# Kernel optimization log

Measured on AMD Instinct MI355X. Metric: run time of the kernel, lower is better.

## Reference

```python
import jax, jax.numpy as jnp
import numpy as np

G, K_ORD = 5, 3          # efficient-kan defaults: grid_size=5, spline_order=3
NB = G + K_ORD           # 8 spline basis functions per input feature
H, NH, S, B = 1024, 16, 1024, 2
HD = H // NH
DFF, E, TOPK = 1024, 4, 2


def b_splines(x):
    # x: [..., in] -> bases: [..., in, NB]; uniform grid on [-1,1] extended by K_ORD knots
    h = 2.0 / G
    grid = jnp.arange(-K_ORD, G + K_ORD + 1, dtype=x.dtype) * h - 1.0  # [G+2k+1]=12
    xg = x[..., None]
    bases = ((xg >= grid[:-1]) & (xg < grid[1:])).astype(x.dtype)      # order-0
    for j in range(1, K_ORD + 1):  # Cox-de Boor recursion
        left = (xg - grid[:-(j + 1)]) / (grid[j:-1] - grid[:-(j + 1)]) * bases[..., :-1]
        right = (grid[j + 1:] - xg) / (grid[j + 1:] - grid[1:-j]) * bases[..., 1:]
        bases = left + right
    return bases  # [..., in, NB]


def kan_linear(x, base_w, spline_w, scaler):
    # base path: SiLU(x) @ W_base^T ; spline path: B(x) contracted with scaled spline weights
    base = jax.nn.silu(x) @ base_w.T                       # [..., out]
    sw = spline_w * scaler[..., None]                      # [out, in, NB]
    spline = jnp.einsum('...ic,oic->...o', b_splines(x), sw)
    return base + spline


def rmsnorm(x, w, eps=1e-6):
    return w * (x * jax.lax.rsqrt(jnp.mean(x * x, axis=-1, keepdims=True) + eps))


def ffn(x, b1, s1, c1, b2, s2, c2, b3, s3, c3):
    # linear3(linear1(x) * linear2(x)), all KANLinear
    return kan_linear(kan_linear(x, b1, s1, c1) * kan_linear(x, b2, s2, c2), b3, s3, c3)


def setup_inputs() -> dict:
    key = jax.random.key(0)
    ks = jax.random.split(key, 24)
    sc = 0.02
    d = {}
    d['x'] = jax.random.normal(ks[0], (B, S, H), jnp.float32)
    inv_freq = 1.0 / (10000.0 ** (np.arange(0, HD, 2, dtype=np.float32) / HD))
    ang = np.arange(S, dtype=np.float32)[:, None] * inv_freq[None, :]  # [S, HD//2]
    d['rot_cos'] = jnp.asarray(np.cos(ang))
    d['rot_sin'] = jnp.asarray(np.sin(ang))
    d['norm1_w'] = jnp.ones((H,), jnp.float32)
    d['norm2_w'] = jnp.ones((H,), jnp.float32)
    d['qkv_base'] = jax.random.normal(ks[1], (3 * H, H), jnp.float32) * sc
    d['qkv_spline'] = jax.random.normal(ks[2], (3 * H, H, NB), jnp.float32) * sc
    d['qkv_scaler'] = jax.random.normal(ks[3], (3 * H, H), jnp.float32) * sc + 1.0
    d['out_w'] = jax.random.normal(ks[4], (H, H), jnp.float32) * sc
    d['out_b'] = jnp.zeros((H,), jnp.float32)
    d['gate_w'] = jax.random.normal(ks[5], (E, H), jnp.float32) * sc
    # stacked expert params (vmapped over E)
    d['w1_base'] = jax.random.normal(ks[6], (E, DFF, H), jnp.float32) * sc
    d['w1_spline'] = jax.random.normal(ks[7], (E, DFF, H, NB), jnp.float32) * sc
    d['w1_scaler'] = jax.random.normal(ks[8], (E, DFF, H), jnp.float32) * sc + 1.0
    d['w2_base'] = jax.random.normal(ks[9], (E, DFF, H), jnp.float32) * sc
    d['w2_spline'] = jax.random.normal(ks[10], (E, DFF, H, NB), jnp.float32) * sc
    d['w2_scaler'] = jax.random.normal(ks[11], (E, DFF, H), jnp.float32) * sc + 1.0
    d['w3_base'] = jax.random.normal(ks[12], (E, H, DFF), jnp.float32) * sc
    d['w3_spline'] = jax.random.normal(ks[13], (E, H, DFF, NB), jnp.float32) * sc
    d['w3_scaler'] = jax.random.normal(ks[14], (E, H, DFF), jnp.float32) * sc + 1.0
    return d


def reference(x, rot_cos, rot_sin, norm1_w, norm2_w, qkv_base, qkv_spline, qkv_scaler,
              out_w, out_b, gate_w, w1_base, w1_spline, w1_scaler, w2_base, w2_spline,
              w2_scaler, w3_base, w3_spline, w3_scaler):
    b, s, h = x.shape
    # ---- attention branch ----
    hn = rmsnorm(x, norm1_w)
    qkv = kan_linear(hn, qkv_base, qkv_spline, qkv_scaler)          # [B,S,3H]
    qkv = qkv.reshape(b, s, NH, 3 * HD).transpose(0, 2, 1, 3)       # [B,NH,S,3HD]
    q, k, v = jnp.split(qkv, 3, axis=-1)                            # [B,NH,S,HD]

    def rope(t):
        tr = t.reshape(b, NH, s, HD // 2, 2)
        re, im = tr[..., 0], tr[..., 1]
        c, sn = rot_cos[:s], rot_sin[:s]                            # [S,HD//2]
        nre = re * c - im * sn
        nim = re * sn + im * c
        return jnp.stack([nre, nim], axis=-1).reshape(b, NH, s, HD)

    q, k = rope(q), rope(k)
    scores = jnp.einsum('bhqd,bhkd->bhqk', q, k) / (HD ** 0.5)
    attn = jax.nn.softmax(scores, axis=-1)
    ctx = jnp.einsum('bhqk,bhkd->bhqd', attn, v)
    ctx = ctx.transpose(0, 2, 1, 3).reshape(b, s, h)
    x = x + ctx @ out_w.T + out_b

    # ---- MoE-KAN FFN branch ----
    h2 = rmsnorm(x, norm2_w)
    gate_logits = h2 @ gate_w.T                                     # [B,S,E]
    w_top, sel = jax.lax.top_k(gate_logits, TOPK)                   # [B,S,K]
    w_top = jax.nn.softmax(w_top.astype(jnp.float32), axis=-1).astype(x.dtype)
    # run every expert densely (same math as masked dispatch), then gather top-k
    y_all = jax.vmap(
        lambda b1, s1, c1, b2, s2, c2, b3, s3, c3:
            ffn(h2, b1, s1, c1, b2, s2, c2, b3, s3, c3)
    )(w1_base, w1_spline, w1_scaler, w2_base, w2_spline, w2_scaler,
      w3_base, w3_spline, w3_scaler)                                # [E,B,S,H]
    y_bseh = jnp.transpose(y_all, (1, 2, 0, 3))                     # [B,S,E,H]
    gathered = jnp.take_along_axis(y_bseh, sel[..., None], axis=2)  # [B,S,K,H]
    moe_out = jnp.sum(w_top[..., None] * gathered, axis=2)          # [B,S,H]
    return x + moe_out
```

## Files before the change

### kernel.cpp

```cpp
#include <hip/hip_runtime.h>
#include <hip/hip_bf16.h>

#define T_TOK 2048
#define H_DIM 1024
#define S_SEQ 1024
#define NHEAD 16
#define E_EXP 4
#define DFF_  1024
#define KAUG  9216

typedef __bf16 bf16x8 __attribute__((ext_vector_type(8)));
typedef float  f32x4  __attribute__((ext_vector_type(4)));
typedef unsigned short ushort_t;

__device__ __forceinline__ float sigmoidf_(float x) { return 1.0f / (1.0f + __expf(-x)); }

__device__ __forceinline__ unsigned short f2bf(float f) {
    unsigned int u = __float_as_uint(f);
    u = (u + 0x7fffu + ((u >> 16) & 1u)) >> 16;
    return (unsigned short)u;
}
__device__ __forceinline__ float bf2f(unsigned short h) {
    return __uint_as_float(((unsigned int)h) << 16);
}

__device__ __forceinline__ void bspline8(float x, float* o) {
    float b[11];
#pragma unroll
    for (int m = 0; m < 11; ++m) {
        float g0 = 0.4f * (float)(m - 3) - 1.0f;
        float g1 = 0.4f * (float)(m - 2) - 1.0f;
        b[m] = (x >= g0 && x < g1) ? 1.0f : 0.0f;
    }
#pragma unroll
    for (int j = 1; j <= 3; ++j) {
        float inv = 1.0f / (0.4f * (float)j);
#pragma unroll
        for (int m = 0; m + j < 11; ++m) {
            float gm   = 0.4f * (float)(m - 3) - 1.0f;
            float gmj1 = 0.4f * (float)(m + j - 2) - 1.0f;
            b[m] = ((x - gm) * b[m] + (gmj1 - x) * b[m + 1]) * inv;
        }
    }
#pragma unroll
    for (int c = 0; c < 8; ++c) o[c] = b[c];
}

__global__ __launch_bounds__(256) void rmsnorm_kernel(const float* __restrict__ x,
                                                      const float* __restrict__ w,
                                                      float* __restrict__ out) {
    long t = blockIdx.x;
    float4 v = ((const float4*)(x + t * H_DIM))[threadIdx.x];
    float ss = v.x * v.x + v.y * v.y + v.z * v.z + v.w * v.w;
#pragma unroll
    for (int m = 1; m < 64; m <<= 1) ss += __shfl_xor(ss, m, 64);
    __shared__ float wsum[4];
    if ((threadIdx.x & 63) == 0) wsum[threadIdx.x >> 6] = ss;
    __syncthreads();
    ss = wsum[0] + wsum[1] + wsum[2] + wsum[3];
    float sc = rsqrtf(ss * (1.0f / (float)H_DIM) + 1e-6f);
    float4 wv = ((const float4*)w)[threadIdx.x];
    float4 r;
    r.x = v.x * sc * wv.x; r.y = v.y * sc * wv.y;
    r.z = v.z * sc * wv.z; r.w = v.w * sc * wv.w;
    ((float4*)(out + t * H_DIM))[threadIdx.x] = r;
}

__global__ __launch_bounds__(256) void pack_act(const float* __restrict__ act,
                                                ushort_t* __restrict__ hi,
                                                ushort_t* __restrict__ lo) {
    long idx = (long)blockIdx.x * 256 + threadIdx.x;
    long m = idx >> 10; int i = (int)(idx & 1023);
    float v = act[idx];
    float ch[9];
    ch[0] = v * sigmoidf_(v);
    bspline8(v, ch + 1);
    ushort_t* oh = hi + m * (long)KAUG + i;
#pragma unroll
    for (int c = 0; c < 9; ++c) oh[(long)c * 1024] = f2bf(ch[c]);
    if (lo) {
        ushort_t* ol = lo + m * (long)KAUG + i;
#pragma unroll
        for (int c = 0; c < 9; ++c) {
            unsigned short h = f2bf(ch[c]);
            ol[(long)c * 1024] = f2bf(ch[c] - bf2f(h));
        }
    }
}

__global__ __launch_bounds__(256) void pack_w(const float* __restrict__ base,
                                              const float* __restrict__ spl,
                                              const float* __restrict__ scal,
                                              ushort_t* __restrict__ hi,
                                              ushort_t* __restrict__ lo,
                                              long total) {
    long idx = (long)blockIdx.x * 256 + threadIdx.x;
    if (idx >= total) return;
    long n = idx >> 10; int i = (int)(idx & 1023);
    float sc = scal[idx];
    const float4* s4 = (const float4*)(spl + idx * 8);
    float4 s0 = s4[0], s1 = s4[1];
    float ch[9] = {base[idx], s0.x * sc, s0.y * sc, s0.z * sc, s0.w * sc,
                   s1.x * sc, s1.y * sc, s1.z * sc, s1.w * sc};
    ushort_t* oh = hi + n * (long)KAUG + i;
#pragma unroll
    for (int c = 0; c < 9; ++c) oh[(long)c * 1024] = f2bf(ch[c]);
    if (lo) {
        ushort_t* ol = lo + n * (long)KAUG + i;
#pragma unroll
        for (int c = 0; c < 9; ++c) {
            unsigned short h = f2bf(ch[c]);
            ol[(long)c * 1024] = f2bf(ch[c] - bf2f(h));
        }
    }
}

__global__ __launch_bounds__(256) void mul_pack4(const float* __restrict__ g1,
                                                 const float* __restrict__ g2,
                                                 ushort_t* __restrict__ G) {
    long idx = (long)blockIdx.x * 256 + threadIdx.x;
    long t = idx >> 12; int ei = (int)(idx & 4095);
    int e = ei >> 10, i = ei & 1023;
    float v = g1[idx] * g2[idx];
    float ch[9];
    ch[0] = v * sigmoidf_(v);
    bspline8(v, ch + 1);
    ushort_t* oh = G + ((long)e * T_TOK + t) * (long)KAUG + i;
#pragma unroll
    for (int c = 0; c < 9; ++c) oh[(long)c * 1024] = f2bf(ch[c]);
}

__global__ __launch_bounds__(256) void split_pack(const float* __restrict__ in,
                                                  ushort_t* __restrict__ hi,
                                                  ushort_t* __restrict__ lo, long n) {
    long i = (long)blockIdx.x * 256 + threadIdx.x;
    if (i >= n) return;
    float v = in[i];
    unsigned short h = f2bf(v);
    hi[i] = h;
    lo[i] = f2bf(v - bf2f(h));
}

#define GLD(gp, lp) __builtin_amdgcn_global_load_lds( \
    (const __attribute__((address_space(1))) void*)(gp), \
    (__attribute__((address_space(3))) void*)(lp), 16, 0, 0)

template<int BM, int SPLIT, int MODE>
__global__ __launch_bounds__(256) void mfma_gemm2(const ushort_t* __restrict__ Ah,
                                                  const ushort_t* __restrict__ Al,
                                                  const ushort_t* __restrict__ Bh,
                                                  const ushort_t* __restrict__ Bl,
                                                  float* __restrict__ C,
                                                  const float* __restrict__ rowScale,
                                                  const float* __restrict__ bias,
                                                  const float* __restrict__ res,
                                                  int N, int K) {
    constexpr int NM = BM / 32;
    __shared__ __align__(16) ushort_t AsH[BM * 32];
    __shared__ __align__(16) ushort_t BsH[128 * 32];
    __shared__ __align__(16) ushort_t AsL[SPLIT ? BM * 32 : 16];
    __shared__ __align__(16) ushort_t BsL[SPLIT ? 128 * 32 : 16];
    const int nx = gridDim.x;
    const int nwg = nx * gridDim.y;
    const int bid = blockIdx.y * nx + blockIdx.x;
    const int q8 = nwg >> 3, r8 = nwg & 7;
    const int xc = bid & 7, dd = bid >> 3;
    const int nid = (xc < r8 ? xc * (q8 + 1) : r8 * (q8 + 1) + (xc - r8) * q8) + dd;
    const int bm = (nid / nx) * BM, bn = (nid % nx) * 128;

    const ushort_t* Ap = Ah;
    const ushort_t* Bp = Bh;
    const float* rsp = rowScale;
    if constexpr (MODE == 3) {
        Ap  += (size_t)blockIdx.z * (size_t)gridDim.y * BM * (size_t)K;
        Bp  += (size_t)blockIdx.z * (size_t)N * (size_t)K;
        rsp += blockIdx.z;
    }

    const int tid = threadIdx.x;
    const int w = tid >> 6, l = tid & 63;
    const int wr = w >> 1, wc = w & 1;
    const int half = l >> 4, lr = l & 15;
    const size_t rb = (size_t)K * 2;

    const int rowB0 = w * 32 + (l >> 2), rowB1 = rowB0 + 16;
    const int cch = l & 3;
    const char* gB0 = (const char*)Bp + (size_t)(bn + rowB0) * rb + ((cch ^ (rowB0 & 3)) * 16);
    const char* gB1 = (const char*)Bp + (size_t)(bn + rowB1) * rb + ((cch ^ (rowB1 & 3)) * 16);
    const char* gB0l = SPLIT ? (const char*)Bl + (size_t)(bn + rowB0) * rb + ((cch ^ (rowB0 & 3)) * 16) : nullptr;
    const char* gB1l = SPLIT ? (const char*)Bl + (size_t)(bn + rowB1) * rb + ((cch ^ (rowB1 & 3)) * 16) : nullptr;
    int rowA0, rowA1;
    if constexpr (BM == 128) { rowA0 = w * 32 + (l >> 2); rowA1 = rowA0 + 16; }
    else                     { rowA0 = w * 16 + (l >> 2); rowA1 = 0; }
    const char* gA0 = (const char*)Ap + (size_t)(bm + rowA0) * rb + ((cch ^ (rowA0 & 3)) * 16);
    const char* gA1 = (BM == 128) ? (const char*)Ap + (size_t)(bm + rowA1) * rb + ((cch ^ (rowA1 & 3)) * 16) : nullptr;
    const char* gA0l = SPLIT ? (const char*)Al + (size_t)(bm + rowA0) * rb + ((cch ^ (rowA0 & 3)) * 16) : nullptr;
    const char* gA1l = (SPLIT && BM == 128) ? (const char*)Al + (size_t)(bm + rowA1) * rb + ((cch ^ (rowA1 & 3)) * 16) : nullptr;

    f32x4 acc[NM][4] = {};
    for (int k0 = 0; k0 < K; k0 += 32) {
        const size_t kb = (size_t)k0 * 2;
        GLD(gA0 + kb, (char*)AsH + ((BM == 128) ? w * 2048 : w * 1024) + l * 16);
        if constexpr (BM == 128) GLD(gA1 + kb, (char*)AsH + w * 2048 + 1024 + l * 16);
        GLD(gB0 + kb, (char*)BsH + w * 2048 + l * 16);
        GLD(gB1 + kb, (char*)BsH + w * 2048 + 1024 + l * 16);
        if constexpr (SPLIT) {
            GLD(gA0l + kb, (char*)AsL + ((BM == 128) ? w * 2048 : w * 1024) + l * 16);
            if constexpr (BM == 128) GLD(gA1l + kb, (char*)AsL + w * 2048 + 1024 + l * 16);
            GLD(gB0l + kb, (char*)BsL + w * 2048 + l * 16);
            GLD(gB1l + kb, (char*)BsL + w * 2048 + 1024 + l * 16);
        }
        __syncthreads();
        bf16x8 ah[NM], bh[4];
#pragma unroll
        for (int mi = 0; mi < NM; ++mi) {
            int r = wr * (BM / 2) + mi * 16 + lr;
            ah[mi] = *(const bf16x8*)((const char*)AsH + r * 64 + ((half ^ (r & 3)) * 16));
        }
#pragma unroll
        for (int ni = 0; ni < 4; ++ni) {
            int r = wc * 64 + ni * 16 + lr;
            bh[ni] = *(const bf16x8*)((const char*)BsH + r * 64 + ((half ^ (r & 3)) * 16));
        }
#pragma unroll
        for (int mi = 0; mi < NM; ++mi)
#pragma unroll
            for (int ni = 0; ni < 4; ++ni)
                acc[mi][ni] = __builtin_amdgcn_mfma_f32_16x16x32_bf16(ah[mi], bh[ni],
                                                                      acc[mi][ni], 0, 0, 0);
        if constexpr (SPLIT) {
            bf16x8 al[NM], bl[4];
#pragma unroll
            for (int mi = 0; mi < NM; ++mi) {
                int r = wr * (BM / 2) + mi * 16 + lr;
                al[mi] = *(const bf16x8*)((const char*)AsL + r * 64 + ((half ^ (r & 3)) * 16));
            }
#pragma unroll
            for (int ni = 0; ni < 4; ++ni) {
                int r = wc * 64 + ni * 16 + lr;
                bl[ni] = *(const bf16x8*)((const char*)BsL + r * 64 + ((half ^ (r & 3)) * 16));
            }
#pragma unroll
            for (int mi = 0; mi < NM; ++mi)
#pragma unroll
                for (int ni = 0; ni < 4; ++ni) {
                    acc[mi][ni] = __builtin_amdgcn_mfma_f32_16x16x32_bf16(ah[mi], bl[ni],
                                                                          acc[mi][ni], 0, 0, 0);
                    acc[mi][ni] = __builtin_amdgcn_mfma_f32_16x16x32_bf16(al[mi], bh[ni],
                                                                          acc[mi][ni], 0, 0, 0);
                }
        }
        __syncthreads();
    }
#pragma unroll
    for (int mi = 0; mi < NM; ++mi)
#pragma unroll
        for (int r = 0; r < 4; ++r) {
            int row = bm + wr * (BM / 2) + mi * 16 + half * 4 + r;
            float rs = (MODE == 1 || MODE == 3) ? rsp[(size_t)row * 4] : 0.0f;
#pragma unroll
            for (int ni = 0; ni < 4; ++ni) {
                int col = bn + wc * 64 + ni * 16 + lr;
                size_t ix = (size_t)row * N + col;
                if constexpr (MODE == 0)      C[ix] = acc[mi][ni][r];
                else if constexpr (MODE == 1) C[ix] += rs * acc[mi][ni][r];
                else if constexpr (MODE == 2) C[ix] = res[ix] + bias[col] + acc[mi][ni][r];
                else                          unsafeAtomicAdd(&C[ix], rs * acc[mi][ni][r]);
            }
        }
}

__global__ __launch_bounds__(256) void qk_pack(const float* __restrict__ qkv,
                                               const float* __restrict__ cs,
                                               const float* __restrict__ sn,
                                               ushort_t* __restrict__ Qh, ushort_t* __restrict__ Ql,
                                               ushort_t* __restrict__ Kh, ushort_t* __restrict__ Kl) {
    int idx = blockIdx.x * 256 + threadIdx.x;
    int p = idx & 31;
    int h = (idx >> 5) & 15;
    int s = (idx >> 9) & (S_SEQ - 1);
    int b = idx >> 19;
    float c = cs[s * 32 + p], si = sn[s * 32 + p];
    long base = ((long)(b * S_SEQ + s)) * 3072 + h * 192;
    long dst = (((long)(b * NHEAD + h)) * S_SEQ + s) * 64 + 2 * p;
    float re = qkv[base + 2 * p], im = qkv[base + 2 * p + 1];
    float qre = (re * c - im * si) * 0.125f;
    float qim = (re * si + im * c) * 0.125f;
    unsigned short hh = f2bf(qre);
    Qh[dst] = hh; Ql[dst] = f2bf(qre - bf2f(hh));
    hh = f2bf(qim);
    Qh[dst + 1] = hh; Ql[dst + 1] = f2bf(qim - bf2f(hh));
    re = qkv[base + 64 + 2 * p]; im = qkv[base + 64 + 2 * p + 1];
    float kre = re * c - im * si;
    float kim = re * si + im * c;
    hh = f2bf(kre);
    Kh[dst] = hh; Kl[dst] = f2bf(kre - bf2f(hh));
    hh = f2bf(kim);
    Kh[dst + 1] = hh; Kl[dst + 1] = f2bf(kim - bf2f(hh));
}

__global__ __launch_bounds__(256) void v_trans(const float* __restrict__ qkv,
                                               ushort_t* __restrict__ Vth,
                                               ushort_t* __restrict__ Vtl) {
    __shared__ float t[64][65];
    const int s0 = blockIdx.x * 64, h = blockIdx.y, b = blockIdx.z;
    const int tid = threadIdx.x;
#pragma unroll
    for (int i = 0; i < 16; ++i) {
        int e = tid + i * 256;
        int sl = e >> 6, d = e & 63;
        t[d][sl] = qkv[((long)(b * S_SEQ + s0 + sl)) * 3072 + h * 192 + 128 + d];
    }
    __syncthreads();
#pragma unroll
    for (int i = 0; i < 16; ++i) {
        int e = tid + i * 256;
        int d = e >> 6, sl = e & 63;
        float v = t[d][sl];
        long o = (((long)(b * NHEAD + h)) * 64 + d) * S_SEQ + s0 + sl;
        unsigned short hh = f2bf(v);
        Vth[o] = hh;
        Vtl[o] = f2bf(v - bf2f(hh));
    }
}

__device__ __forceinline__ bf16x8 lds_frag(const ushort_t* base, int row, int chunk) {
    return *(const bf16x8*)((const char*)base + row * 128 + ((chunk ^ (row & 7)) * 16));
}

__global__ __launch_bounds__(256) void attn_mfma(const ushort_t* __restrict__ Qh,
                                                 const ushort_t* __restrict__ Ql,
                                                 const ushort_t* __restrict__ Kh,
                                                 const ushort_t* __restrict__ Kl,
                                                 const ushort_t* __restrict__ Vth,
                                                 const ushort_t* __restrict__ Vtl,
                                                 float* __restrict__ ctx) {
    __shared__ __align__(16) ushort_t KsH[64 * 64], KsL[64 * 64];
    __shared__ __align__(16) ushort_t VsH[64 * 64], VsL[64 * 64];
    __shared__ __align__(16) ushort_t Ps[4][2][16][72];
    const int qb = blockIdx.x * 64, h = blockIdx.y, b = blockIdx.z;
    const int tid = threadIdx.x;
    const int w = tid >> 6, l = tid & 63;
    const int lr = l & 15, g = l >> 4;
    const long bh = b * NHEAD + h;

    const long qoff = (bh * S_SEQ + qb + w * 16 + lr) * 64 + g * 8;
    bf16x8 qh0 = *(const bf16x8*)(Qh + qoff);
    bf16x8 qh1 = *(const bf16x8*)(Qh + qoff + 32);
    bf16x8 ql0 = *(const bf16x8*)(Ql + qoff);
    bf16x8 ql1 = *(const bf16x8*)(Ql + qoff + 32);

    const int rowS0 = w * 16 + (l >> 3), rowS1 = rowS0 + 8;
    const int cch = l & 7;
    const char* gK0 = (const char*)Kh + (bh * S_SEQ + rowS0) * 128 + ((cch ^ (rowS0 & 7)) * 16);
    const char* gK1 = (const char*)Kh + (bh * S_SEQ + rowS1) * 128 + ((cch ^ (rowS1 & 7)) * 16);
    const char* gKl0 = (const char*)Kl + (bh * S_SEQ + rowS0) * 128 + ((cch ^ (rowS0 & 7)) * 16);
    const char* gKl1 = (const char*)Kl + (bh * S_SEQ + rowS1) * 128 + ((cch ^ (rowS1 & 7)) * 16);
    const char* gV0 = (const char*)Vth + (bh * 64 + rowS0) * 2048 + ((cch ^ (rowS0 & 7)) * 16);
    const char* gV1 = (const char*)Vth + (bh * 64 + rowS1) * 2048 + ((cch ^ (rowS1 & 7)) * 16);
    const char* gVl0 = (const char*)Vtl + (bh * 64 + rowS0) * 2048 + ((cch ^ (rowS0 & 7)) * 16);
    const char* gVl1 = (const char*)Vtl + (bh * 64 + rowS1) * 2048 + ((cch ^ (rowS1 & 7)) * 16);

    float m_run[4] = {-1e30f, -1e30f, -1e30f, -1e30f};
    float l_run[4] = {0.f, 0.f, 0.f, 0.f};
    f32x4 acco[4] = {};

    for (int k0 = 0; k0 < S_SEQ; k0 += 64) {
        GLD(gK0 + (size_t)k0 * 128, (char*)KsH + w * 2048 + l * 16);
        GLD(gK1 + (size_t)k0 * 128, (char*)KsH + w * 2048 + 1024 + l * 16);
        GLD(gKl0 + (size_t)k0 * 128, (char*)KsL + w * 2048 + l * 16);
        GLD(gKl1 + (size_t)k0 * 128, (char*)KsL + w * 2048 + 1024 + l * 16);
        GLD(gV0 + (size_t)k0 * 2, (char*)VsH + w * 2048 + l * 16);
        GLD(gV1 + (size_t)k0 * 2, (char*)VsH + w * 2048 + 1024 + l * 16);
        GLD(gVl0 + (size_t)k0 * 2, (char*)VsL + w * 2048 + l * 16);
        GLD(gVl1 + (size_t)k0 * 2, (char*)VsL + w * 2048 + 1024 + l * 16);
        __syncthreads();

        f32x4 accs[4] = {};
#pragma unroll
        for (int n = 0; n < 4; ++n) {
            bf16x8 bkh0 = lds_frag(KsH, n * 16 + lr, g);
            bf16x8 bkh1 = lds_frag(KsH, n * 16 + lr, g + 4);
            bf16x8 bkl0 = lds_frag(KsL, n * 16 + lr, g);
            bf16x8 bkl1 = lds_frag(KsL, n * 16 + lr, g + 4);
            accs[n] = __builtin_amdgcn_mfma_f32_16x16x32_bf16(qh0, bkh0, accs[n], 0, 0, 0);
            accs[n] = __builtin_amdgcn_mfma_f32_16x16x32_bf16(qh1, bkh1, accs[n], 0, 0, 0);
            accs[n] = __builtin_amdgcn_mfma_f32_16x16x32_bf16(qh0, bkl0, accs[n], 0, 0, 0);
            accs[n] = __builtin_amdgcn_mfma_f32_16x16x32_bf16(qh1, bkl1, accs[n], 0, 0, 0);
            accs[n] = __builtin_amdgcn_mfma_f32_16x16x32_bf16(ql0, bkh0, accs[n], 0, 0, 0);
            accs[n] = __builtin_amdgcn_mfma_f32_16x16x32_bf16(ql1, bkh1, accs[n], 0, 0, 0);
        }
        float alpha[4];
#pragma unroll
        for (int r = 0; r < 4; ++r) {
            float mx = fmaxf(fmaxf(accs[0][r], accs[1][r]), fmaxf(accs[2][r], accs[3][r]));
#pragma unroll
            for (int msk = 1; msk < 16; msk <<= 1) mx = fmaxf(mx, __shfl_xor(mx, msk, 64));
            float m_new = fmaxf(m_run[r], mx);
            float ps = 0.f;
#pragma unroll
            for (int n = 0; n < 4; ++n) {
                float p = __expf(accs[n][r] - m_new);
                accs[n][r] = p;
                ps += p;
            }
#pragma unroll
            for (int msk = 1; msk < 16; msk <<= 1) ps += __shfl_xor(ps, msk, 64);
            alpha[r] = __expf(m_run[r] - m_new);
            l_run[r] = l_run[r] * alpha[r] + ps;
            m_run[r] = m_new;
        }
#pragma unroll
        for (int nd = 0; nd < 4; ++nd)
#pragma unroll
            for (int r = 0; r < 4; ++r) acco[nd][r] *= alpha[r];
#pragma unroll
        for (int n = 0; n < 4; ++n)
#pragma unroll
            for (int r = 0; r < 4; ++r) {
                float p = accs[n][r];
                unsigned short hh = f2bf(p);
                Ps[w][0][g * 4 + r][n * 16 + lr] = hh;
                Ps[w][1][g * 4 + r][n * 16 + lr] = f2bf(p - bf2f(hh));
            }
        __syncthreads();
        bf16x8 pah0 = *(const bf16x8*)&Ps[w][0][lr][g * 8];
        bf16x8 pah1 = *(const bf16x8*)&Ps[w][0][lr][32 + g * 8];
        bf16x8 pal0 = *(const bf16x8*)&Ps[w][1][lr][g * 8];
        bf16x8 pal1 = *(const bf16x8*)&Ps[w][1][lr][32 + g * 8];
#pragma unroll
        for (int nd = 0; nd < 4; ++nd) {
            bf16x8 bvh0 = lds_frag(VsH, nd * 16 + lr, g);
            bf16x8 bvh1 = lds_frag(VsH, nd * 16 + lr, g + 4);
            bf16x8 bvl0 = lds_frag(VsL, nd * 16 + lr, g);
            bf16x8 bvl1 = lds_frag(VsL, nd * 16 + lr, g + 4);
            acco[nd] = __builtin_amdgcn_mfma_f32_16x16x32_bf16(pah0, bvh0, acco[nd], 0, 0, 0);
            acco[nd] = __builtin_amdgcn_mfma_f32_16x16x32_bf16(pah1, bvh1, acco[nd], 0, 0, 0);
            acco[nd] = __builtin_amdgcn_mfma_f32_16x16x32_bf16(pah0, bvl0, acco[nd], 0, 0, 0);
            acco[nd] = __builtin_amdgcn_mfma_f32_16x16x32_bf16(pah1, bvl1, acco[nd], 0, 0, 0);
            acco[nd] = __builtin_amdgcn_mfma_f32_16x16x32_bf16(pal0, bvh0, acco[nd], 0, 0, 0);
            acco[nd] = __builtin_amdgcn_mfma_f32_16x16x32_bf16(pal1, bvh1, acco[nd], 0, 0, 0);
        }
        __syncthreads();
    }
#pragma unroll
    for (int r = 0; r < 4; ++r) {
        float inv = 1.0f / l_run[r];
        long row = (long)b * S_SEQ + qb + w * 16 + g * 4 + r;
#pragma unroll
        for (int nd = 0; nd < 4; ++nd)
            ctx[row * H_DIM + h * 64 + nd * 16 + lr] = acco[nd][r] * inv;
    }
}

__global__ __launch_bounds__(256) void gate_kernel(const float* __restrict__ h2,
                                                   const float* __restrict__ gate_w,
                                                   float* __restrict__ gw) {
    long t = blockIdx.x;
    float sum[4] = {0, 0, 0, 0};
    for (int i = threadIdx.x; i < H_DIM; i += 256) {
        float v = h2[t * H_DIM + i];
#pragma unroll
        for (int e = 0; e < 4; ++e) sum[e] = fmaf(v, gate_w[e * H_DIM + i], sum[e]);
    }
#pragma unroll
    for (int w = 1; w < 64; w <<= 1)
#pragma unroll
        for (int e = 0; e < 4; ++e) sum[e] += __shfl_xor(sum[e], w, 64);
    __shared__ float part[4][4];
    if ((threadIdx.x & 63) == 0)
#pragma unroll
        for (int e = 0; e < 4; ++e) part[e][threadIdx.x >> 6] = sum[e];
    __syncthreads();
    if (threadIdx.x == 0) {
        float lg[4];
#pragma unroll
        for (int e = 0; e < 4; ++e) lg[e] = part[e][0] + part[e][1] + part[e][2] + part[e][3];
        int i0 = 0;
        for (int e = 1; e < 4; ++e) if (lg[e] > lg[i0]) i0 = e;
        int i1 = -1;
        for (int e = 0; e < 4; ++e) if (e != i0 && (i1 < 0 || lg[e] > lg[i1])) i1 = e;
        float mx = fmaxf(lg[i0], lg[i1]);
        float e0 = __expf(lg[i0] - mx), e1 = __expf(lg[i1] - mx);
        float inv = 1.0f / (e0 + e1);
        float o[4] = {0, 0, 0, 0};
        o[i0] = e0 * inv; o[i1] = e1 * inv;
#pragma unroll
        for (int e = 0; e < 4; ++e) gw[t * 4 + e] = o[e];
    }
}

#define KI 8
#define BKK 72
__global__ __launch_bounds__(256) void kan_gemm(const float* __restrict__ Act,
                                                const float* __restrict__ baseW,
                                                const float* __restrict__ splW,
                                                const float* __restrict__ scal,
                                                float* __restrict__ C,
                                                const float* __restrict__ rowScale,
                                                int rsStride, int N, int mode) {
    __shared__ float As[BKK][64];
    __shared__ float Bs[BKK][64];
    const int bm = blockIdx.y * 64;
    const int bn = blockIdx.x * 64;
    const int tid = threadIdx.x;
    const int tx = tid & 15, ty = tid >> 4;
    float acc[4][4] = {};
    for (int i0 = 0; i0 < H_DIM; i0 += KI) {
        for (int e = tid; e < 64 * KI; e += 256) {
            int m = e >> 3, ii = e & 7;
            float xv = Act[(long)(bm + m) * H_DIM + i0 + ii];
            float sp[8];
            bspline8(xv, sp);
            As[ii * 9][m] = xv * sigmoidf_(xv);
#pragma unroll
            for (int c = 0; c < 8; ++c) As[ii * 9 + 1 + c][m] = sp[c];
        }
        for (int e = tid; e < 64 * KI; e += 256) {
            int n = e >> 3, ii = e & 7;
            long w = (long)(bn + n) * H_DIM + i0 + ii;
            float sc = scal[w];
            Bs[ii * 9][n] = baseW[w];
            const float4* sp4 = (const float4*)(splW + w * 8);
            float4 s0 = sp4[0], s1 = sp4[1];
            Bs[ii * 9 + 1][n] = s0.x * sc; Bs[ii * 9 + 2][n] = s0.y * sc;
            Bs[ii * 9 + 3][n] = s0.z * sc; Bs[ii * 9 + 4][n] = s0.w * sc;
            Bs[ii * 9 + 5][n] = s1.x * sc; Bs[ii * 9 + 6][n] = s1.y * sc;
            Bs[ii * 9 + 7][n] = s1.z * sc; Bs[ii * 9 + 8][n] = s1.w * sc;
        }
        __syncthreads();
#pragma unroll 8
        for (int k = 0; k < BKK; ++k) {
            float4 a = *(const float4*)&As[k][ty * 4];
            float4 b = *(const float4*)&Bs[k][tx * 4];
            float av[4] = {a.x, a.y, a.z, a.w};
            float bv[4] = {b.x, b.y, b.z, b.w};
#pragma unroll
            for (int i = 0; i < 4; ++i)
#pragma unroll
                for (int j = 0; j < 4; ++j) acc[i][j] = fmaf(av[i], bv[j], acc[i][j]);
        }
        __syncthreads();
    }
#pragma unroll
    for (int i = 0; i < 4; ++i) {
        long m = bm + ty * 4 + i;
        float rs = (mode == 1) ? rowScale[m * rsStride] : 0.0f;
#pragma unroll
        for (int j = 0; j < 4; ++j) {
            long idx = m * (long)N + bn + tx * 4 + j;
            if (mode == 0) C[idx] = acc[i][j];
            else           C[idx] += rs * acc[i][j];
        }
    }
}

__global__ __launch_bounds__(256) void gemm_bias_res(const float* __restrict__ A,
                                                     const float* __restrict__ Bw,
                                                     const float* __restrict__ bias,
                                                     const float* __restrict__ res,
                                                     float* __restrict__ C) {
    __shared__ float As[16][64];
    __shared__ float Bs[16][64];
    const int bm = blockIdx.y * 64, bn = blockIdx.x * 64;
    const int tid = threadIdx.x;
    const int tx = tid & 15, ty = tid >> 4;
    float acc[4][4] = {};
    for (int k0 = 0; k0 < 1024; k0 += 16) {
        for (int e = tid; e < 1024; e += 256) {
            int r = e >> 4, kk = e & 15;
            As[kk][r] = A[(long)(bm + r) * 1024 + k0 + kk];
            Bs[kk][r] = Bw[(long)(bn + r) * 1024 + k0 + kk];
        }
        __syncthreads();
#pragma unroll
        for (int k = 0; k < 16; ++k) {
            float4 a = *(const float4*)&As[k][ty * 4];
            float4 b = *(const float4*)&Bs[k][tx * 4];
            float av[4] = {a.x, a.y, a.z, a.w};
            float bv[4] = {b.x, b.y, b.z, b.w};
#pragma unroll
            for (int i = 0; i < 4; ++i)
#pragma unroll
                for (int j = 0; j < 4; ++j) acc[i][j] = fmaf(av[i], bv[j], acc[i][j]);
        }
        __syncthreads();
    }
#pragma unroll
    for (int i = 0; i < 4; ++i) {
        long m = bm + ty * 4 + i;
#pragma unroll
        for (int j = 0; j < 4; ++j) {
            long n = bn + tx * 4 + j;
            C[m * 1024 + n] = res[m * 1024 + n] + bias[n] + acc[i][j];
        }
    }
}

__global__ __launch_bounds__(256) void rope_kernel(float* __restrict__ qkv,
                                                   const float* __restrict__ cs,
                                                   const float* __restrict__ sn) {
    int idx = blockIdx.x * 256 + threadIdx.x;
    if (idx >= T_TOK * NHEAD * 32) return;
    int p = idx & 31;
    int n = (idx >> 5) & 15;
    int t = idx >> 9;
    int s = t & (S_SEQ - 1);
    float c = cs[s * 32 + p], si = sn[s * 32 + p];
    long base = (long)t * 3072 + n * 192;
    float re = qkv[base + 2 * p], im = qkv[base + 2 * p + 1];
    qkv[base + 2 * p]     = re * c - im * si;
    qkv[base + 2 * p + 1] = re * si + im * c;
    re = qkv[base + 64 + 2 * p]; im = qkv[base + 64 + 2 * p + 1];
    qkv[base + 64 + 2 * p]     = re * c - im * si;
    qkv[base + 64 + 2 * p + 1] = re * si + im * c;
}

__global__ __launch_bounds__(256) void attn_kernel(const float* __restrict__ qkv,
                                                   float* __restrict__ ctx) {
    const int qb = blockIdx.x * 32;
    const int h = blockIdx.y, b = blockIdx.z;
    __shared__ float Qs[32][64];
    __shared__ float Ks[64][64];
    __shared__ float Vs[64][64];
    __shared__ float Ss[32][64];
    const int tid = threadIdx.x;
    const int q = tid >> 3, g = tid & 7;
    for (int e = tid; e < 32 * 64; e += 256) {
        int r = e >> 6, d = e & 63;
        Qs[r][d] = qkv[(long)(b * S_SEQ + qb + r) * 3072 + h * 192 + d];
    }
    float m_run = -1e30f, l_run = 0.0f;
    float acc[8] = {};
    for (int k0 = 0; k0 < S_SEQ; k0 += 64) {
        for (int e = tid; e < 64 * 64; e += 256) {
            int r = e >> 6, d = e & 63;
            long base = (long)(b * S_SEQ + k0 + r) * 3072 + h * 192;
            Ks[r][d] = qkv[base + 64 + d];
            Vs[r][d] = qkv[base + 128 + d];
        }
        __syncthreads();
        float s[8];
#pragma unroll
        for (int kk = 0; kk < 8; ++kk) {
            int k = g * 8 + kk;
            float dot = 0.0f;
#pragma unroll
            for (int d = 0; d < 64; ++d) dot = fmaf(Qs[q][d], Ks[k][d], dot);
            s[kk] = dot * 0.125f;
        }
        float mx = s[0];
#pragma unroll
        for (int kk = 1; kk < 8; ++kk) mx = fmaxf(mx, s[kk]);
#pragma unroll
        for (int w = 1; w < 8; w <<= 1) mx = fmaxf(mx, __shfl_xor(mx, w, 64));
        float m_new = fmaxf(m_run, mx);
        float p[8], ls = 0.0f;
#pragma unroll
        for (int kk = 0; kk < 8; ++kk) { p[kk] = __expf(s[kk] - m_new); ls += p[kk]; }
#pragma unroll
        for (int w = 1; w < 8; w <<= 1) ls += __shfl_xor(ls, w, 64);
        float alpha = __expf(m_run - m_new);
        l_run = l_run * alpha + ls;
        m_run = m_new;
#pragma unroll
        for (int kk = 0; kk < 8; ++kk) Ss[q][g * 8 + kk] = p[kk];
        __syncthreads();
#pragma unroll
        for (int j = 0; j < 8; ++j) acc[j] *= alpha;
        for (int k = 0; k < 64; ++k) {
            float pv = Ss[q][k];
#pragma unroll
            for (int j = 0; j < 8; ++j) acc[j] = fmaf(pv, Vs[k][g * 8 + j], acc[j]);
        }
        __syncthreads();
    }
    float inv = 1.0f / l_run;
#pragma unroll
    for (int j = 0; j < 8; ++j)
        ctx[(long)(b * S_SEQ + qb + q) * H_DIM + h * 64 + g * 8 + j] = acc[j] * inv;
}

__global__ __launch_bounds__(256) void mul_kernel(const float* __restrict__ a,
                                                  const float* __restrict__ b,
                                                  float* __restrict__ c, int n) {
    int i = blockIdx.x * 256 + threadIdx.x;
    if (i < n) c[i] = a[i] * b[i];
}

extern "C" void kernel_launch(void* const* d_in, const int* in_sizes, int n_in,
                              void* d_out, int out_size, void* d_ws, size_t ws_size,
                              hipStream_t stream) {
    const float* x          = (const float*)d_in[0];
    const float* rot_cos    = (const float*)d_in[1];
    const float* rot_sin    = (const float*)d_in[2];
    const float* norm1_w    = (const float*)d_in[3];
    const float* norm2_w    = (const float*)d_in[4];
    const float* qkv_base   = (const float*)d_in[5];
    const float* qkv_spline = (const float*)d_in[6];
    const float* qkv_scaler = (const float*)d_in[7];
    const float* out_w      = (const float*)d_in[8];
    const float* out_b      = (const float*)d_in[9];
    const float* gate_w     = (const float*)d_in[10];
    const float* w1_base    = (const float*)d_in[11];
    const float* w1_spline  = (const float*)d_in[12];
    const float* w1_scaler  = (const float*)d_in[13];
    const float* w2_base    = (const float*)d_in[14];
    const float* w2_spline  = (const float*)d_in[15];
    const float* w2_scaler  = (const float*)d_in[16];
    const float* w3_base    = (const float*)d_in[17];
    const float* w3_spline  = (const float*)d_in[18];
    const float* w3_scaler  = (const float*)d_in[19];
    float* out = (float*)d_out;

    const size_t SZ_AUG  = (size_t)T_TOK * KAUG * 2;
    const size_t SZ_WQ   = (size_t)3072 * KAUG * 2;
    const size_t SZ_QKV  = (size_t)T_TOK * 3072 * 4;
    const size_t SZ_G12  = (size_t)T_TOK * 2048 * 4;
    const size_t SZ_TOK  = (size_t)T_TOK * H_DIM * 4;
    const size_t NEED = 2 * SZ_AUG + 2 * SZ_WQ + SZ_QKV + SZ_G12 + 2 * SZ_TOK + 32768;

    if (ws_size >= NEED) {
        char* pool = (char*)d_ws;
        ushort_t* A_hi = (ushort_t*)pool;
        ushort_t* A_lo = (ushort_t*)(pool + SZ_AUG);
        char* W1p = pool + 2 * SZ_AUG;
        char* W2p = pool + 2 * SZ_AUG + SZ_WQ;
        float* qkv = (float*)(pool + 2 * SZ_AUG + 2 * SZ_WQ);
        float* ctx = (float*)(pool + 2 * SZ_AUG + 2 * SZ_WQ + SZ_QKV + SZ_G12);
        float* tok = (float*)(pool + 2 * SZ_AUG + 2 * SZ_WQ + SZ_QKV + SZ_G12 + SZ_TOK);
        float* gw  = (float*)(pool + NEED - 32768);
        ushort_t* W1b = (ushort_t*)W1p;
        ushort_t* W2b = (ushort_t*)W2p;
        const size_t SZ_P = (size_t)T_TOK * 1024 * 2;
        ushort_t* Qh  = (ushort_t*)W1p;
        ushort_t* Ql  = (ushort_t*)(W1p + SZ_P);
        ushort_t* Kh  = (ushort_t*)(W1p + 2 * SZ_P);
        ushort_t* Kl  = (ushort_t*)(W1p + 3 * SZ_P);
        ushort_t* Vth = (ushort_t*)(W1p + 4 * SZ_P);
        ushort_t* Vtl = (ushort_t*)(W1p + 5 * SZ_P);
        ushort_t* CtxH = (ushort_t*)W2p;
        ushort_t* CtxL = (ushort_t*)(W2p + SZ_P);
        ushort_t* OWh  = (ushort_t*)(W2p + 2 * SZ_P);
        ushort_t* OWl  = (ushort_t*)(W2p + 2 * SZ_P + SZ_P / 2);
        const size_t SZ_G4 = (size_t)T_TOK * 4096 * 4;
        ushort_t* A2   = (ushort_t*)pool;
        ushort_t* W12  = (ushort_t*)(pool + SZ_AUG);
        float*    g1a  = (float*)(pool + NEED - 32768 - 2 * SZ_G4);
        float*    g2a  = (float*)(pool + NEED - 32768 - SZ_G4);
        ushort_t* Gall = (ushort_t*)pool;
        ushort_t* W3a  = (ushort_t*)(pool + 4 * SZ_AUG);

        rmsnorm_kernel<<<T_TOK, 256, 0, stream>>>(x, norm1_w, tok);
        pack_act<<<(T_TOK * 1024) / 256, 256, 0, stream>>>(tok, A_hi, A_lo);
        pack_w<<<(3072 * 1024) / 256, 256, 0, stream>>>(qkv_base, qkv_spline, qkv_scaler,
                                                        W1b, W2b, (long)3072 * 1024);
        mfma_gemm2<128, 1, 0><<<dim3(3072 / 128, T_TOK / 128), 256, 0, stream>>>(
            A_hi, A_lo, W1b, W2b, qkv, nullptr, nullptr, nullptr, 3072, KAUG);
        qk_pack<<<(T_TOK * NHEAD * 32) / 256, 256, 0, stream>>>(qkv, rot_cos, rot_sin,
                                                                Qh, Ql, Kh, Kl);
        v_trans<<<dim3(S_SEQ / 64, NHEAD, 2), 256, 0, stream>>>(qkv, Vth, Vtl);
        attn_mfma<<<dim3(S_SEQ / 64, NHEAD, 2), 256, 0, stream>>>(Qh, Ql, Kh, Kl,
                                                                  Vth, Vtl, ctx);
        split_pack<<<(T_TOK * 1024) / 256, 256, 0, stream>>>(ctx, CtxH, CtxL,
                                                             (long)T_TOK * 1024);
        split_pack<<<(1024 * 1024) / 256, 256, 0, stream>>>(out_w, OWh, OWl,
                                                            (long)1024 * 1024);
        mfma_gemm2<128, 1, 2><<<dim3(1024 / 128, T_TOK / 128), 256, 0, stream>>>(
            CtxH, CtxL, OWh, OWl, out, nullptr, out_b, x, 1024, 1024);
        rmsnorm_kernel<<<T_TOK, 256, 0, stream>>>(out, norm2_w, tok);
        gate_kernel<<<T_TOK, 256, 0, stream>>>(tok, gate_w, gw);

        pack_act<<<(T_TOK * 1024) / 256, 256, 0, stream>>>(tok, A2, nullptr);
        pack_w<<<(4 * 1024 * 1024) / 256, 256, 0, stream>>>(
            w1_base, w1_spline, w1_scaler, W12, nullptr, (long)4 * 1024 * 1024);
        mfma_gemm2<128, 0, 0><<<dim3(4096 / 128, T_TOK / 128), 256, 0, stream>>>(
            A2, nullptr, W12, nullptr, g1a, nullptr, nullptr, nullptr, 4096, KAUG);
        pack_w<<<(4 * 1024 * 1024) / 256, 256, 0, stream>>>(
            w2_base, w2_spline, w2_scaler, W12, nullptr, (long)4 * 1024 * 1024);
        mfma_gemm2<128, 0, 0><<<dim3(4096 / 128, T_TOK / 128), 256, 0, stream>>>(
            A2, nullptr, W12, nullptr, g2a, nullptr, nullptr, nullptr, 4096, KAUG);
        mul_pack4<<<(T_TOK * 4096) / 256, 256, 0, stream>>>(g1a, g2a, Gall);
        pack_w<<<(4 * 1024 * 1024) / 256, 256, 0, stream>>>(
            w3_base, w3_spline, w3_scaler, W3a, nullptr, (long)4 * 1024 * 1024);
        mfma_gemm2<128, 0, 3><<<dim3(1024 / 128, T_TOK / 128, E_EXP), 256, 0, stream>>>(
            Gall, nullptr, W3a, nullptr, out, gw, nullptr, nullptr, 1024, KAUG);
        return;
    }

    char* ws = (char*)d_ws;
    float* hn  = (float*)ws; ws += (size_t)T_TOK * H_DIM * 4;
    float* qkv = (float*)ws; ws += (size_t)T_TOK * 3072 * 4;
    float* ctx = (float*)ws; ws += (size_t)T_TOK * H_DIM * 4;
    float* h2  = (float*)ws; ws += (size_t)T_TOK * H_DIM * 4;
    float* gw  = (float*)ws; ws += (size_t)T_TOK * E_EXP * 4;
    float* g1  = (float*)ws; ws += (size_t)T_TOK * DFF_ * 4;
    float* g2  = (float*)ws; ws += (size_t)T_TOK * DFF_ * 4;
    float* gm  = (float*)ws; ws += (size_t)T_TOK * DFF_ * 4;

    rmsnorm_kernel<<<T_TOK, 256, 0, stream>>>(x, norm1_w, hn);
    dim3 gq(3072 / 64, T_TOK / 64);
    kan_gemm<<<gq, 256, 0, stream>>>(hn, qkv_base, qkv_spline, qkv_scaler, qkv,
                                     nullptr, 0, 3072, 0);
    rope_kernel<<<(T_TOK * NHEAD * 32) / 256, 256, 0, stream>>>(qkv, rot_cos, rot_sin);
    dim3 ga(S_SEQ / 32, NHEAD, 2);
    attn_kernel<<<ga, 256, 0, stream>>>(qkv, ctx);
    dim3 go(1024 / 64, T_TOK / 64);
    gemm_bias_res<<<go, 256, 0, stream>>>(ctx, out_w, out_b, x, out);
    rmsnorm_kernel<<<T_TOK, 256, 0, stream>>>(out, norm2_w, h2);
    gate_kernel<<<T_TOK, 256, 0, stream>>>(h2, gate_w, gw);
    dim3 ge(1024 / 64, T_TOK / 64);
    for (int e = 0; e < E_EXP; ++e) {
        long wo = (long)e * DFF_ * H_DIM;
        kan_gemm<<<ge, 256, 0, stream>>>(h2, w1_base + wo, w1_spline + wo * 8,
                                         w1_scaler + wo, g1, nullptr, 0, DFF_, 0);
        kan_gemm<<<ge, 256, 0, stream>>>(h2, w2_base + wo, w2_spline + wo * 8,
                                         w2_scaler + wo, g2, nullptr, 0, DFF_, 0);
        mul_kernel<<<(T_TOK * DFF_) / 256, 256, 0, stream>>>(g1, g2, gm, T_TOK * DFF_);
        kan_gemm<<<ge, 256, 0, stream>>>(gm, w3_base + wo, w3_spline + wo * 8,
                                         w3_scaler + wo, out, gw + e, E_EXP, H_DIM, 1);
    }
}
```

Measured before the change: 1.588 ms.

## Split-K GEMMs with atomics, merge W1/W2 GEMM with bf16 output

Adds a KSPLIT template parameter so the QKV, out-projection and expert-W3 GEMMs split the K dimension across grid z and accumulate with atomic adds. This raises workgroup counts on the small-N GEMMs, which underfill the GPU. The W1 and W2 expert GEMMs are merged into one N=8192 launch that writes bf16 outputs, and mul_pack4 reads those bf16 values, halving intermediate traffic. The XCD-aware block remapping is removed, and a prefill kernel plus a memset replace the fused bias/residual epilogue. The costs are atomic traffic, extra zero/prefill passes and bf16 rounding of the g1/g2 intermediates.

```diff
diff --git a/kernel.cpp b/kernel.cpp
--- a/kernel.cpp
+++ b/kernel.cpp
@@ -64,6 +64,17 @@
     r.x = v.x * sc * wv.x; r.y = v.y * sc * wv.y;
     r.z = v.z * sc * wv.z; r.w = v.w * sc * wv.w;
     ((float4*)(out + t * H_DIM))[threadIdx.x] = r;
+}
+
+__global__ __launch_bounds__(256) void prefill_out(const float* __restrict__ x,
+                                                   const float* __restrict__ bias,
+                                                   float* __restrict__ out) {
+    long i = (long)blockIdx.x * 256 + threadIdx.x;
+    float4 xv = ((const float4*)x)[i];
+    float4 bv = ((const float4*)bias)[i & 255];
+    float4 r;
+    r.x = xv.x + bv.x; r.y = xv.y + bv.y; r.z = xv.z + bv.z; r.w = xv.w + bv.w;
+    ((float4*)out)[i] = r;
 }
 
 __global__ __launch_bounds__(256) void pack_act(const float* __restrict__ act,
@@ -115,13 +126,14 @@
     }
 }
 
-__global__ __launch_bounds__(256) void mul_pack4(const float* __restrict__ g1,
-                                                 const float* __restrict__ g2,
+__global__ __launch_bounds__(256) void mul_pack4(const ushort_t* __restrict__ g12,
                                                  ushort_t* __restrict__ G) {
     long idx = (long)blockIdx.x * 256 + threadIdx.x;
     long t = idx >> 12; int ei = (int)(idx & 4095);
     int e = ei >> 10, i = ei & 1023;
-    float v = g1[idx] * g2[idx];
+    float g1 = bf2f(g12[t * 8192 + ei]);
+    float g2 = bf2f(g12[t * 8192 + 4096 + ei]);
+    float v = g1 * g2;
     float ch[9];
     ch[0] = v * sigmoidf_(v);
     bspline8(v, ch + 1);
@@ -145,37 +157,32 @@
     (const __attribute__((address_space(1))) void*)(gp), \
     (__attribute__((address_space(3))) void*)(lp), 16, 0, 0)
 
-template<int BM, int SPLIT, int MODE>
+template<int BM, int SPLIT, int MODE, int KSPLIT>
 __global__ __launch_bounds__(256) void mfma_gemm2(const ushort_t* __restrict__ Ah,
                                                   const ushort_t* __restrict__ Al,
                                                   const ushort_t* __restrict__ Bh,
                                                   const ushort_t* __restrict__ Bl,
                                                   float* __restrict__ C,
                                                   const float* __restrict__ rowScale,
-                                                  const float* __restrict__ bias,
-                                                  const float* __restrict__ res,
                                                   int N, int K) {
     constexpr int NM = BM / 32;
     __shared__ __align__(16) ushort_t AsH[BM * 32];
     __shared__ __align__(16) ushort_t BsH[128 * 32];
     __shared__ __align__(16) ushort_t AsL[SPLIT ? BM * 32 : 16];
     __shared__ __align__(16) ushort_t BsL[SPLIT ? 128 * 32 : 16];
-    const int nx = gridDim.x;
-    const int nwg = nx * gridDim.y;
-    const int bid = blockIdx.y * nx + blockIdx.x;
-    const int q8 = nwg >> 3, r8 = nwg & 7;
-    const int xc = bid & 7, dd = bid >> 3;
-    const int nid = (xc < r8 ? xc * (q8 + 1) : r8 * (q8 + 1) + (xc - r8) * q8) + dd;
-    const int bm = (nid / nx) * BM, bn = (nid % nx) * 128;
-
-    const ushort_t* Ap = Ah;
-    const ushort_t* Bp = Bh;
-    const float* rsp = rowScale;
-    if constexpr (MODE == 3) {
-        Ap  += (size_t)blockIdx.z * (size_t)gridDim.y * BM * (size_t)K;
-        Bp  += (size_t)blockIdx.z * (size_t)N * (size_t)K;
-        rsp += blockIdx.z;
-    }
+    const int bm = blockIdx.y * BM, bn = blockIdx.x * 128;
+
+    const int KC = K / KSPLIT;
+    int e = 0, kk = 0;
+    if constexpr (MODE == 3) { e = blockIdx.z / KSPLIT; kk = blockIdx.z % KSPLIT; }
+    else if constexpr (KSPLIT > 1) { kk = blockIdx.z; }
+    const ushort_t* Ap = Ah + (MODE == 3 ? (size_t)e * (size_t)gridDim.y * BM * K : 0)
+                            + (size_t)kk * KC;
+    const ushort_t* Bp = Bh + (MODE == 3 ? (size_t)e * (size_t)N * K : 0)
+                            + (size_t)kk * KC;
+    const ushort_t* Alp = SPLIT ? Al + (size_t)kk * KC : nullptr;
+    const ushort_t* Blp = SPLIT ? Bl + (size_t)kk * KC : nullptr;
+    const float* rsp = rowScale + (MODE == 3 ? e : 0);
 
     const int tid = threadIdx.x;
     const int w = tid >> 6, l = tid & 63;
@@ -187,18 +194,18 @@
     const int cch = l & 3;
     const char* gB0 = (const char*)Bp + (size_t)(bn + rowB0) * rb + ((cch ^ (rowB0 & 3)) * 16);
     const char* gB1 = (const char*)Bp + (size_t)(bn + rowB1) * rb + ((cch ^ (rowB1 & 3)) * 16);
-    const char* gB0l = SPLIT ? (const char*)Bl + (size_t)(bn + rowB0) * rb + ((cch ^ (rowB0 & 3)) * 16) : nullptr;
-    const char* gB1l = SPLIT ? (const char*)Bl + (size_t)(bn + rowB1) * rb + ((cch ^ (rowB1 & 3)) * 16) : nullptr;
+    const char* gB0l = SPLIT ? (const char*)Blp + (size_t)(bn + rowB0) * rb + ((cch ^ (rowB0 & 3)) * 16) : nullptr;
+    const char* gB1l = SPLIT ? (const char*)Blp + (size_t)(bn + rowB1) * rb + ((cch ^ (rowB1 & 3)) * 16) : nullptr;
     int rowA0, rowA1;
     if constexpr (BM == 128) { rowA0 = w * 32 + (l >> 2); rowA1 = rowA0 + 16; }
     else                     { rowA0 = w * 16 + (l >> 2); rowA1 = 0; }
     const char* gA0 = (const char*)Ap + (size_t)(bm + rowA0) * rb + ((cch ^ (rowA0 & 3)) * 16);
     const char* gA1 = (BM == 128) ? (const char*)Ap + (size_t)(bm + rowA1) * rb + ((cch ^ (rowA1 & 3)) * 16) : nullptr;
-    const char* gA0l = SPLIT ? (const char*)Al + (size_t)(bm + rowA0) * rb + ((cch ^ (rowA0 & 3)) * 16) : nullptr;
-    const char* gA1l = (SPLIT && BM == 128) ? (const char*)Al + (size_t)(bm + rowA1) * rb + ((cch ^ (rowA1 & 3)) * 16) : nullptr;
+    const char* gA0l = SPLIT ? (const char*)Alp + (size_t)(bm + rowA0) * rb + ((cch ^ (rowA0 & 3)) * 16) : nullptr;
+    const char* gA1l = (SPLIT && BM == 128) ? (const char*)Alp + (size_t)(bm + rowA1) * rb + ((cch ^ (rowA1 & 3)) * 16) : nullptr;
 
     f32x4 acc[NM][4] = {};
-    for (int k0 = 0; k0 < K; k0 += 32) {
+    for (int k0 = 0; k0 < KC; k0 += 32) {
         const size_t kb = (size_t)k0 * 2;
         GLD(gA0 + kb, (char*)AsH + ((BM == 128) ? w * 2048 : w * 1024) + l * 16);
         if constexpr (BM == 128) GLD(gA1 + kb, (char*)AsH + w * 2048 + 1024 + l * 16);
@@ -257,15 +264,15 @@
 #pragma unroll
         for (int r = 0; r < 4; ++r) {
             int row = bm + wr * (BM / 2) + mi * 16 + half * 4 + r;
-            float rs = (MODE == 1 || MODE == 3) ? rsp[(size_t)row * 4] : 0.0f;
+            float rs = (MODE == 3) ? rsp[(size_t)row * 4] : 0.0f;
 #pragma unroll
             for (int ni = 0; ni < 4; ++ni) {
                 int col = bn + wc * 64 + ni * 16 + lr;
                 size_t ix = (size_t)row * N + col;
                 if constexpr (MODE == 0)      C[ix] = acc[mi][ni][r];
-                else if constexpr (MODE == 1) C[ix] += rs * acc[mi][ni][r];
-                else if constexpr (MODE == 2) C[ix] = res[ix] + bias[col] + acc[mi][ni][r];
-                else                          unsafeAtomicAdd(&C[ix], rs * acc[mi][ni][r]);
+                else if constexpr (MODE == 3) unsafeAtomicAdd(&C[ix], rs * acc[mi][ni][r]);
+                else if constexpr (MODE == 5) unsafeAtomicAdd(&C[ix], acc[mi][ni][r]);
+                else                          ((ushort_t*)C)[ix] = f2bf(acc[mi][ni][r]);
             }
         }
 }
@@ -743,11 +750,10 @@
         ushort_t* CtxL = (ushort_t*)(W2p + SZ_P);
         ushort_t* OWh  = (ushort_t*)(W2p + 2 * SZ_P);
         ushort_t* OWl  = (ushort_t*)(W2p + 2 * SZ_P + SZ_P / 2);
-        const size_t SZ_G4 = (size_t)T_TOK * 4096 * 4;
+        const size_t SZ_W12 = (size_t)8192 * KAUG * 2;
         ushort_t* A2   = (ushort_t*)pool;
         ushort_t* W12  = (ushort_t*)(pool + SZ_AUG);
-        float*    g1a  = (float*)(pool + NEED - 32768 - 2 * SZ_G4);
-        float*    g2a  = (float*)(pool + NEED - 32768 - SZ_G4);
+        ushort_t* g12  = (ushort_t*)(pool + SZ_AUG + SZ_W12);
         ushort_t* Gall = (ushort_t*)pool;
         ushort_t* W3a  = (ushort_t*)(pool + 4 * SZ_AUG);
 
@@ -755,8 +761,9 @@
         pack_act<<<(T_TOK * 1024) / 256, 256, 0, stream>>>(tok, A_hi, A_lo);
         pack_w<<<(3072 * 1024) / 256, 256, 0, stream>>>(qkv_base, qkv_spline, qkv_scaler,
                                                         W1b, W2b, (long)3072 * 1024);
-        mfma_gemm2<128, 1, 0><<<dim3(3072 / 128, T_TOK / 128), 256, 0, stream>>>(
-            A_hi, A_lo, W1b, W2b, qkv, nullptr, nullptr, nullptr, 3072, KAUG);
+        hipMemsetAsync(qkv, 0, SZ_QKV, stream);
+        mfma_gemm2<128, 1, 5, 4><<<dim3(3072 / 128, T_TOK / 128, 4), 256, 0, stream>>>(
+            A_hi, A_lo, W1b, W2b, qkv, nullptr, 3072, KAUG);
         qk_pack<<<(T_TOK * NHEAD * 32) / 256, 256, 0, stream>>>(qkv, rot_cos, rot_sin,
                                                                 Qh, Ql, Kh, Kl);
         v_trans<<<dim3(S_SEQ / 64, NHEAD, 2), 256, 0, stream>>>(qkv, Vth, Vtl);
@@ -766,25 +773,25 @@
                                                              (long)T_TOK * 1024);
         split_pack<<<(1024 * 1024) / 256, 256, 0, stream>>>(out_w, OWh, OWl,
                                                             (long)1024 * 1024);
-        mfma_gemm2<128, 1, 2><<<dim3(1024 / 128, T_TOK / 128), 256, 0, stream>>>(
-            CtxH, CtxL, OWh, OWl, out, nullptr, out_b, x, 1024, 1024);
+        prefill_out<<<(T_TOK * H_DIM / 4) / 256, 256, 0, stream>>>(x, out_b, out);
+        mfma_gemm2<128, 1, 5, 4><<<dim3(1024 / 128, T_TOK / 128, 4), 256, 0, stream>>>(
+            CtxH, CtxL, OWh, OWl, out, nullptr, 1024, 1024);
         rmsnorm_kernel<<<T_TOK, 256, 0, stream>>>(out, norm2_w, tok);
         gate_kernel<<<T_TOK, 256, 0, stream>>>(tok, gate_w, gw);
 
         pack_act<<<(T_TOK * 1024) / 256, 256, 0, stream>>>(tok, A2, nullptr);
         pack_w<<<(4 * 1024 * 1024) / 256, 256, 0, stream>>>(
             w1_base, w1_spline, w1_scaler, W12, nullptr, (long)4 * 1024 * 1024);
-        mfma_gemm2<128, 0, 0><<<dim3(4096 / 128, T_TOK / 128), 256, 0, stream>>>(
-            A2, nullptr, W12, nullptr, g1a, nullptr, nullptr, nullptr, 4096, KAUG);
         pack_w<<<(4 * 1024 * 1024) / 256, 256, 0, stream>>>(
-            w2_base, w2_spline, w2_scaler, W12, nullptr, (long)4 * 1024 * 1024);
-        mfma_gemm2<128, 0, 0><<<dim3(4096 / 128, T_TOK / 128), 256, 0, stream>>>(
-            A2, nullptr, W12, nullptr, g2a, nullptr, nullptr, nullptr, 4096, KAUG);
-        mul_pack4<<<(T_TOK * 4096) / 256, 256, 0, stream>>>(g1a, g2a, Gall);
+            w2_base, w2_spline, w2_scaler, W12 + (size_t)4096 * KAUG, nullptr,
+            (long)4 * 1024 * 1024);
+        mfma_gemm2<128, 0, 6, 1><<<dim3(8192 / 128, T_TOK / 128), 256, 0, stream>>>(
+            A2, nullptr, W12, nullptr, (float*)g12, nullptr, 8192, KAUG);
+        mul_pack4<<<(T_TOK * 4096) / 256, 256, 0, stream>>>(g12, Gall);
         pack_w<<<(4 * 1024 * 1024) / 256, 256, 0, stream>>>(
             w3_base, w3_spline, w3_scaler, W3a, nullptr, (long)4 * 1024 * 1024);
-        mfma_gemm2<128, 0, 3><<<dim3(1024 / 128, T_TOK / 128, E_EXP), 256, 0, stream>>>(
-            Gall, nullptr, W3a, nullptr, out, gw, nullptr, nullptr, 1024, KAUG);
+        mfma_gemm2<128, 0, 3, 2><<<dim3(1024 / 128, T_TOK / 128, E_EXP * 2), 256, 0, stream>>>(
+            Gall, nullptr, W3a, nullptr, out, gw, 1024, KAUG);
         return;
     }
 
```

New measurement: 1.490 ms. 6.1% less time.
